# Optimization experiments

Hardware: AMD Instinct MI355X
Metric: run time of the kernel (lower is better)

## Reference

```python
import jax, jax.numpy as jnp
import numpy as np

N_NODES = 100000
N_EDGES = 1600000
IN_C, HID_C, OUT_C = 128, 128, 64


def gcn_conv(x, src, dst, W, b, num_nodes):
    # PyG GCNConv: add self-loops, symmetric normalization, linear transform,
    # aggregate source features into targets.
    h = x @ W  # [N, C_out]
    loop = jnp.arange(num_nodes, dtype=src.dtype)
    s = jnp.concatenate([src, loop])
    d = jnp.concatenate([dst, loop])
    deg = jax.ops.segment_sum(jnp.ones_like(d, dtype=h.dtype), d, num_segments=num_nodes)
    inv_sqrt = jnp.where(deg > 0, jax.lax.rsqrt(deg), 0.0)
    norm = inv_sqrt[s] * inv_sqrt[d]  # [E+N]
    msgs = h[s] * norm[:, None]  # gather + scale
    out = jax.ops.segment_sum(msgs, d, num_segments=num_nodes)  # scatter-add
    return out + b


def setup_inputs() -> dict:
    key = jax.random.key(0)
    k1, k2, k3, k4 = jax.random.split(key, 4)
    x = jax.random.normal(k1, (N_NODES, IN_C), dtype=jnp.float32)
    edge_index = jax.random.randint(k2, (2, N_EDGES), 0, N_NODES, dtype=jnp.int64)
    W1 = jax.random.normal(k3, (IN_C, HID_C), dtype=jnp.float32) * (1.0 / np.sqrt(IN_C))
    b1 = jnp.zeros((HID_C,), dtype=jnp.float32)
    W2 = jax.random.normal(k4, (HID_C, OUT_C), dtype=jnp.float32) * (1.0 / np.sqrt(HID_C))
    b2 = jnp.zeros((OUT_C,), dtype=jnp.float32)
    return {"x": x, "edge_index": edge_index, "W1": W1, "b1": b1, "W2": W2, "b2": b2}


def reference(x, edge_index, W1, b1, W2, b2):
    num_nodes = x.shape[0]
    src, dst = edge_index[0], edge_index[1]  # PyG flow: source -> target
    h = gcn_conv(x, src, dst, W1, b1, num_nodes)
    h = jax.nn.relu(h)  # dropout is identity in eval mode
    out = gcn_conv(h, src, dst, W2, b2, num_nodes)
    return out
```

## Files before the change

kernel.cpp:

```cpp
#include <hip/hip_runtime.h>

#define IN_C 128
#define HID_C 128
#define OUT_C 64

#define BSPAN 256
#define BCAP  5120
#define NBMAX 512
#define ACHUNK 4096

typedef unsigned int uint32;
typedef unsigned short ushort16;
typedef _Float16 f16;
typedef f16   f16x8 __attribute__((ext_vector_type(8)));
typedef float f32x4 __attribute__((ext_vector_type(4)));


__device__ __forceinline__ ushort16 f2bf(float f) {
    union { float f; uint32 u; } v; v.f = f;
    uint32 r = v.u + 0x7FFFu + ((v.u >> 16) & 1u);
    return (ushort16)(r >> 16);
}

__device__ __forceinline__ void unpack2(uint32 u, float& f0, float& f1) {
    union { uint32 x; float f; } a, b;
    a.x = u << 16;
    b.x = u & 0xFFFF0000u;
    f0 = a.f; f1 = b.f;
}

__device__ __forceinline__ void acc_row(uint4 r, float* acc) {
    float f0, f1;
    unpack2(r.x, f0, f1); acc[0] += f0; acc[1] += f1;
    unpack2(r.y, f0, f1); acc[2] += f0; acc[3] += f1;
    unpack2(r.z, f0, f1); acc[4] += f0; acc[5] += f1;
    unpack2(r.w, f0, f1); acc[6] += f0; acc[7] += f1;
}


__launch_bounds__(256)
__global__ void bin_edges_kernel(const int* __restrict__ src, const int* __restrict__ dst,
                                 int* __restrict__ bucketCur, uint32* __restrict__ binned,
                                 int* __restrict__ deg, int E, int nbuck) {
    __shared__ int hist[NBMAX];
    __shared__ int base[NBMAX];
    const int tid = threadIdx.x;
    const int e0  = blockIdx.x * ACHUNK;

    for (int i = tid; i < NBMAX; i += 256) hist[i] = 0;
    __syncthreads();

    int d[16], s[16], rk[16];
#pragma unroll
    for (int j = 0; j < 16; j++) {
        int e = e0 + j * 256 + tid;
        if (e < E) {
            d[j] = dst[e];
            s[j] = src[e];
            rk[j] = atomicAdd(&hist[d[j] >> 8], 1);
            atomicAdd(&deg[d[j]], 1);
        } else d[j] = -1;
    }
    __syncthreads();

    for (int b = tid; b < nbuck; b += 256) {
        int h = hist[b];
        base[b] = h ? atomicAdd(&bucketCur[b], h) : 0;
    }
    __syncthreads();

#pragma unroll
    for (int j = 0; j < 16; j++) {
        if (d[j] >= 0) {
            int b = d[j] >> 8;
            int pos = base[b] + rk[j];
            if (pos < BCAP)
                binned[(size_t)b * BCAP + pos] =
                    ((uint32)(d[j] & 255) << 17) | (uint32)s[j];
        }
    }
}


template <int C>
__device__ __forceinline__ void wprep_one(const float* __restrict__ W, f16* __restrict__ Wf, int t) {
    constexpr int NCT = C / 16;
    int lane = t & 63;
    int ctkc = t >> 6;
    int ct = ctkc % NCT, kc = ctkc / NCT;
    int kbase = kc * 32 + (lane >> 4) * 8;
    int col   = ct * 16 + (lane & 15);
    f16 v[8];
#pragma unroll
    for (int j = 0; j < 8; j++) v[j] = (f16)W[(size_t)(kbase + j) * C + col];
    *(uint4*)(Wf + (size_t)t * 8) = *(const uint4*)v;
}

__global__ void wprep_both(const float* __restrict__ W1, f16* __restrict__ Wf1,
                           const float* __restrict__ W2, f16* __restrict__ Wf2,
                           int* __restrict__ bucketCur, int* __restrict__ deg,
                           int nbuck, int N) {
    constexpr int T1 = 4 * (HID_C / 16) * 64;
    constexpr int T2 = 4 * (OUT_C / 16) * 64;
    int t = blockIdx.x * 256 + threadIdx.x;
    if (t < nbuck) bucketCur[t] = 0;
    if (t < N)     deg[t] = 0;
    if (t < T1)            wprep_one<HID_C>(W1, Wf1, t);
    else if (t < T1 + T2)  wprep_one<OUT_C>(W2, Wf2, t - T1);
}


__launch_bounds__(256)
__global__ void csr_and_gemm(const uint32* __restrict__ binned, const int* __restrict__ bucketCur,
                             int* __restrict__ csr_src, int* __restrict__ rowbeg,
                             int* __restrict__ rowend, float* __restrict__ inv,
                             const float* __restrict__ X, const f16* __restrict__ Wf,
                             const int* __restrict__ deg, ushort16* __restrict__ outb,
                             int N, int ncsr) {
    __shared__ __align__(16) char smem[49152];
    const int tid = threadIdx.x;

    if ((int)blockIdx.x < ncsr) {
        constexpr int MAXIT = BCAP / 256;
        int* cnt  = (int*)smem;
        int* scn  = cnt + BSPAN;
        int* excl = scn + BSPAN;
        const int b   = blockIdx.x;
        const int n0  = b * BSPAN;
        const int ne  = min(bucketCur[b], BCAP);
        const uint32* bp = binned + (size_t)b * BCAP;

        cnt[tid] = 0;
        __syncthreads();

        uint32 ebuf[MAXIT];
        int    rbuf[MAXIT];
        int nmine = 0;
        for (int i = tid; i < ne; i += 256) {
            uint32 e = bp[i];
            ebuf[nmine] = e;
            rbuf[nmine] = atomicAdd(&cnt[e >> 17], 1);
            nmine++;
        }
        __syncthreads();

        int v = cnt[tid];
        scn[tid] = v;
        __syncthreads();
        for (int off = 1; off < 256; off <<= 1) {
            int u = (tid >= off) ? scn[tid - off] : 0;
            __syncthreads();
            scn[tid] += u;
            __syncthreads();
        }
        int ex = scn[tid] - v;
        excl[tid] = ex;

        int n = n0 + tid;
        if (n < N) {
            int gb = b * BCAP + ex;
            rowbeg[n] = gb;
            rowend[n] = gb + v;
            inv[n] = rsqrtf((float)(v + 1));
        }
        __syncthreads();

        for (int j = 0; j < nmine; j++) {
            uint32 e = ebuf[j];
            csr_src[(size_t)b * BCAP + excl[e >> 17] + rbuf[j]] = (int)(e & 0x1FFFFu);
        }
    } else {
        constexpr int C = HID_C;
        constexpr int NCT = C / 16;
        f16* As = (f16*)smem;
        f16* Bs = (f16*)(smem + 16384);

        const int lane = tid & 63;
        const int w    = tid >> 6;
        const int row0 = ((int)blockIdx.x - ncsr) * 64;

        {
            constexpr int TOT = 4 * NCT * 64 * 8;
            const uint4* s = (const uint4*)Wf;
            uint4* d = (uint4*)Bs;
#pragma unroll
            for (int i = 0; i < TOT / 8 / 256; i++)
                d[tid + i * 256] = s[tid + i * 256];
        }

        {
            int r   = tid >> 2;
            int seg = tid & 3;
            int row = row0 + r;
            int ws_ = r >> 4;
            int r15 = r & 15;
#pragma unroll
            for (int i = 0; i < 8; i++) {
                int k = seg * 32 + i * 4;
                float4 v = make_float4(0.f, 0.f, 0.f, 0.f);
                if (row < N) v = *(const float4*)(X + (size_t)row * 128 + k);
                int q = (k >> 3) & 3, j0 = k & 7;
                f16 h[4] = {(f16)v.x, (f16)v.y, (f16)v.z, (f16)v.w};
                int slot = ((seg * 4 + ws_) * 64 + (q * 16 + r15)) * 8 + j0;
                *(uint2*)(As + slot) = *(const uint2*)h;
            }
        }
        __syncthreads();

        f32x4 acc[NCT];
#pragma unroll
        for (int c = 0; c < NCT; c++) acc[c] = (f32x4){0.f, 0.f, 0.f, 0.f};
#pragma unroll
        for (int kc = 0; kc < 4; kc++) {
            f16x8 a = *(const f16x8*)&As[((kc * 4 + w) * 64 + lane) * 8];
#pragma unroll
            for (int ct = 0; ct < NCT; ct++) {
                f16x8 b = *(const f16x8*)&Bs[((kc * NCT + ct) * 64 + lane) * 8];
                acc[ct] = __builtin_amdgcn_mfma_f32_16x16x32_f16(a, b, acc[ct], 0, 0, 0);
            }
        }

        __syncthreads();
        ushort16* Ds = (ushort16*)As;
        const int q = lane >> 4;
        float iv[4];
#pragma unroll
        for (int reg = 0; reg < 4; reg++) {
            int row = row0 + w * 16 + q * 4 + reg;
            iv[reg] = (row < N) ? rsqrtf((float)(deg[row] + 1)) : 0.f;
        }
#pragma unroll
        for (int ct = 0; ct < NCT; ct++) {
#pragma unroll
            for (int reg = 0; reg < 4; reg++) {
                int r = w * 16 + q * 4 + reg;
                Ds[r * C + ct * 16 + (lane & 15)] = f2bf(acc[ct][reg] * iv[reg]);
            }
        }
        __syncthreads();
        {
            int r  = tid >> 2;
            int row = row0 + r;
            if (row < N) {
                constexpr int SPT = C / 4;
                int c0 = (tid & 3) * SPT;
                const uint4* s = (const uint4*)&Ds[r * C + c0];
                uint4* d = (uint4*)(outb + (size_t)row * C + c0);
#pragma unroll
                for (int i = 0; i < SPT / 8; i++) d[i] = s[i];
            }
        }
    }
}


__launch_bounds__(512, 4)
__global__ void fused_gather_gemm(const int* __restrict__ rowbeg, const int* __restrict__ rowend,
                                  const int* __restrict__ csr,
                                  const ushort16* __restrict__ hsb,
                                  const float* __restrict__ inv, const float* __restrict__ bias1,
                                  const f16* __restrict__ Wf2,
                                  ushort16* __restrict__ outb, int N) {
    constexpr int CIN = 128, COUT = 64, NCT = COUT / 16;
    __shared__ __align__(16) f16 As[4 * 4 * 64 * 8];
    __shared__ __align__(16) f16 Bs[4 * NCT * 64 * 8];

    const int tid  = threadIdx.x;
    const int lane = tid & 63;
    const int w    = tid >> 6;
    const int row0 = blockIdx.x * 64;

    {
        const uint4* s = (const uint4*)Wf2;
        uint4* d = (uint4*)Bs;
        d[tid]       = s[tid];
        d[tid + 512] = s[tid + 512];
    }

    {
        const int r = tid >> 3;
        const int q = tid & 7;
        const int n = row0 + r;
        float acc[16];
#pragma unroll
        for (int j = 0; j < 16; j++) acc[j] = 0.f;

        if (n < N) {
            {
                const ushort16* base = hsb + (size_t)n * CIN + q * 16;
                uint4 s0 = *(const uint4*)(base);
                uint4 s1 = *(const uint4*)(base + 8);
                acc_row(s0, acc); acc_row(s1, acc + 8);
            }
            const int end = rowend[n];
            int i = rowbeg[n];
            for (; i + 4 <= end; i += 4) {
                const ushort16* p0 = hsb + (size_t)csr[i]     * CIN + q * 16;
                const ushort16* p1 = hsb + (size_t)csr[i + 1] * CIN + q * 16;
                const ushort16* p2 = hsb + (size_t)csr[i + 2] * CIN + q * 16;
                const ushort16* p3 = hsb + (size_t)csr[i + 3] * CIN + q * 16;
                uint4 a0 = *(const uint4*)(p0);
                uint4 a1 = *(const uint4*)(p0 + 8);
                uint4 b0 = *(const uint4*)(p1);
                uint4 b1 = *(const uint4*)(p1 + 8);
                uint4 c0 = *(const uint4*)(p2);
                uint4 c1 = *(const uint4*)(p2 + 8);
                uint4 d0 = *(const uint4*)(p3);
                uint4 d1 = *(const uint4*)(p3 + 8);
                acc_row(a0, acc); acc_row(a1, acc + 8);
                acc_row(b0, acc); acc_row(b1, acc + 8);
                acc_row(c0, acc); acc_row(c1, acc + 8);
                acc_row(d0, acc); acc_row(d1, acc + 8);
            }
            for (; i < end; i++) {
                const ushort16* p0 = hsb + (size_t)csr[i] * CIN + q * 16;
                uint4 a0 = *(const uint4*)(p0);
                uint4 a1 = *(const uint4*)(p0 + 8);
                acc_row(a0, acc); acc_row(a1, acc + 8);
            }

            float iv = inv[n];
#pragma unroll
            for (int j = 0; j < 16; j++)
                acc[j] = fmaxf(fmaf(iv, acc[j], bias1[q * 16 + j]), 0.f);
        }

        const int ws_ = r >> 4, r15 = r & 15;
        const int seg = q >> 1;
#pragma unroll
        for (int u = 0; u < 2; u++) {
            const int i8 = (q & 1) * 2 + u;
            f16 hv[8];
#pragma unroll
            for (int j = 0; j < 8; j++) hv[j] = (f16)acc[u * 8 + j];
            int slot = ((seg * 4 + ws_) * 64 + (i8 * 16 + r15)) * 8;
            *(uint4*)(As + slot) = *(const uint4*)hv;
        }
    }
    __syncthreads();

    f32x4 acc2[NCT];
#pragma unroll
    for (int c = 0; c < NCT; c++) acc2[c] = (f32x4){0.f, 0.f, 0.f, 0.f};
    if (w < 4) {
#pragma unroll
        for (int kc = 0; kc < 4; kc++) {
            f16x8 a = *(const f16x8*)&As[((kc * 4 + w) * 64 + lane) * 8];
#pragma unroll
            for (int ct = 0; ct < NCT; ct++) {
                f16x8 b = *(const f16x8*)&Bs[((kc * NCT + ct) * 64 + lane) * 8];
                acc2[ct] = __builtin_amdgcn_mfma_f32_16x16x32_f16(a, b, acc2[ct], 0, 0, 0);
            }
        }
    }

    __syncthreads();
    ushort16* Ds = (ushort16*)As;
    if (w < 4) {
        const int q2 = lane >> 4;
        float iv2[4];
#pragma unroll
        for (int reg = 0; reg < 4; reg++) {
            int row = row0 + w * 16 + q2 * 4 + reg;
            iv2[reg] = (row < N) ? inv[row] : 0.f;
        }
#pragma unroll
        for (int ct = 0; ct < NCT; ct++) {
#pragma unroll
            for (int reg = 0; reg < 4; reg++) {
                int r = w * 16 + q2 * 4 + reg;
                Ds[r * COUT + ct * 16 + (lane & 15)] = f2bf(acc2[ct][reg] * iv2[reg]);
            }
        }
    }
    __syncthreads();
    {
        const int r   = tid >> 3;
        const int row = row0 + r;
        if (row < N) {
            const int c0 = (tid & 7) * 8;
            *(uint4*)(outb + (size_t)row * COUT + c0) = *(const uint4*)&Ds[r * COUT + c0];
        }
    }
}


template <int C, bool RELU>
__launch_bounds__(256)
__global__ void gather_agg_bf16(const int* __restrict__ rowbeg, const int* __restrict__ rowend,
                                const int* __restrict__ csr_src,
                                const ushort16* __restrict__ hsb, const float* __restrict__ inv,
                                const float* __restrict__ b, float* __restrict__ out, int N) {
    constexpr int TPN = C / 8;
    constexpr int NPB = 256 / TPN;
    int n    = blockIdx.x * NPB + threadIdx.x / TPN;
    int lane = threadIdx.x % TPN;
    if (n >= N) return;
    int c8 = lane * 8;

    float acc[8];
    {
        uint4 raw = *(const uint4*)(hsb + (size_t)n * C + c8);
        unpack2(raw.x, acc[0], acc[1]);
        unpack2(raw.y, acc[2], acc[3]);
        unpack2(raw.z, acc[4], acc[5]);
        unpack2(raw.w, acc[6], acc[7]);
    }

    int beg = rowbeg[n];
    int end = rowend[n];
    int i = beg;
    for (; i + 4 <= end; i += 4) {
        int s0 = csr_src[i];
        int s1 = csr_src[i + 1];
        int s2 = csr_src[i + 2];
        int s3 = csr_src[i + 3];
        uint4 r0 = *(const uint4*)(hsb + (size_t)s0 * C + c8);
        uint4 r1 = *(const uint4*)(hsb + (size_t)s1 * C + c8);
        uint4 r2 = *(const uint4*)(hsb + (size_t)s2 * C + c8);
        uint4 r3 = *(const uint4*)(hsb + (size_t)s3 * C + c8);
        acc_row(r0, acc); acc_row(r1, acc); acc_row(r2, acc); acc_row(r3, acc);
    }
    for (; i < end; i++) {
        uint4 r0 = *(const uint4*)(hsb + (size_t)csr_src[i] * C + c8);
        acc_row(r0, acc);
    }

    float iv = inv[n];
    float4 b0 = *(const float4*)(b + c8);
    float4 b1 = *(const float4*)(b + c8 + 4);
    float r[8];
    r[0] = fmaf(iv, acc[0], b0.x); r[1] = fmaf(iv, acc[1], b0.y);
    r[2] = fmaf(iv, acc[2], b0.z); r[3] = fmaf(iv, acc[3], b0.w);
    r[4] = fmaf(iv, acc[4], b1.x); r[5] = fmaf(iv, acc[5], b1.y);
    r[6] = fmaf(iv, acc[6], b1.z); r[7] = fmaf(iv, acc[7], b1.w);
    if (RELU) {
#pragma unroll
        for (int j = 0; j < 8; j++) r[j] = fmaxf(r[j], 0.f);
    }
    float* po = out + (size_t)n * C + c8;
    *(float4*)(po)     = make_float4(r[0], r[1], r[2], r[3]);
    *(float4*)(po + 4) = make_float4(r[4], r[5], r[6], r[7]);
}

extern "C" void kernel_launch(void* const* d_in, const int* in_sizes, int n_in,
                              void* d_out, int out_size, void* d_ws, size_t ws_size,
                              hipStream_t stream) {
    const float* x  = (const float*)d_in[0];
    const int*   ei = (const int*)d_in[1];
    const float* W1 = (const float*)d_in[2];
    const float* b1 = (const float*)d_in[3];
    const float* W2 = (const float*)d_in[4];
    const float* b2 = (const float*)d_in[5];
    float* out = (float*)d_out;

    const int N = in_sizes[0] / IN_C;
    const int E = in_sizes[1] / 2;
    const int* src = ei;
    const int* dst = ei + E;
    const int nbuck = (N + BSPAN - 1) / BSPAN;

    char* ws = (char*)d_ws;
    auto align_up = [](size_t v) { return (v + 1023) & ~(size_t)1023; };
    size_t off = 0;
    int*      bucketCur = (int*)(ws + off);      off += align_up((size_t)nbuck * sizeof(int));
    int*      deg       = (int*)(ws + off);      off += align_up((size_t)N * sizeof(int));
    float*    inv       = (float*)(ws + off);    off += align_up((size_t)N * sizeof(float));
    int*      rowbeg    = (int*)(ws + off);      off += align_up((size_t)N * sizeof(int));
    int*      rowend    = (int*)(ws + off);      off += align_up((size_t)N * sizeof(int));
    uint32*   binned    = (uint32*)(ws + off);   off += align_up((size_t)nbuck * BCAP * sizeof(uint32));
    int*      csrs      = (int*)(ws + off);      off += align_up((size_t)nbuck * BCAP * sizeof(int));
    f16*      Wf1       = (f16*)(ws + off);      off += align_up((size_t)4 * (HID_C/16) * 64 * 8 * sizeof(f16));
    f16*      Wf2       = (f16*)(ws + off);      off += align_up((size_t)4 * (OUT_C/16) * 64 * 8 * sizeof(f16));
    ushort16* hs1b      = (ushort16*)(ws + off); off += align_up((size_t)N * HID_C * sizeof(ushort16));
    ushort16* hs2b      = (ushort16*)(ws + off); off += align_up((size_t)N * OUT_C * sizeof(ushort16));

    wprep_both<<<(N + 255) / 256, 256, 0, stream>>>(
        W1, Wf1, W2, Wf2, bucketCur, deg, nbuck, N);

    bin_edges_kernel<<<(E + ACHUNK - 1) / ACHUNK, 256, 0, stream>>>(
        src, dst, bucketCur, binned, deg, E, nbuck);

    {
        const int ngemm = (N + 63) / 64;
        csr_and_gemm<<<nbuck + ngemm, 256, 0, stream>>>(
            binned, bucketCur, csrs, rowbeg, rowend, inv,
            x, Wf1, deg, hs1b, N, nbuck);
    }

    fused_gather_gemm<<<(N + 63) / 64, 512, 0, stream>>>(
        rowbeg, rowend, csrs, hs1b, inv, b1, Wf2, hs2b, N);

    {
        constexpr int NPB = 256 / (OUT_C / 8);
        gather_agg_bf16<OUT_C, false><<<(N + NPB - 1) / NPB, 256, 0, stream>>>(
            rowbeg, rowend, csrs, hs2b, inv, b2, out, N);
    }
}
```

Measured before the change: 304.5 us.

## Replace global degree atomics with per-bucket LDS degree count kernel

The edge-binning kernel no longer issues one global atomicAdd per edge into a degree array. A new deg_inv_kernel instead recounts per-node degrees for each 256-node bucket from the binned edges, using shared-memory atomics, and writes inv directly. The GEMM branch now reads that precomputed inv instead of recomputing rsqrt from deg. Weight preparation is folded into extra blocks of the binning kernel, and the bucket counters are zeroed with a memset. The trade is an extra launch and an extra pass over the binned array in exchange for removing scattered global atomics.

```diff
diff --git a/kernel.cpp b/kernel.cpp
--- a/kernel.cpp
+++ b/kernel.cpp
@@ -35,50 +35,6 @@
     unpack2(r.y, f0, f1); acc[2] += f0; acc[3] += f1;
     unpack2(r.z, f0, f1); acc[4] += f0; acc[5] += f1;
     unpack2(r.w, f0, f1); acc[6] += f0; acc[7] += f1;
-}
-
-
-__launch_bounds__(256)
-__global__ void bin_edges_kernel(const int* __restrict__ src, const int* __restrict__ dst,
-                                 int* __restrict__ bucketCur, uint32* __restrict__ binned,
-                                 int* __restrict__ deg, int E, int nbuck) {
-    __shared__ int hist[NBMAX];
-    __shared__ int base[NBMAX];
-    const int tid = threadIdx.x;
-    const int e0  = blockIdx.x * ACHUNK;
-
-    for (int i = tid; i < NBMAX; i += 256) hist[i] = 0;
-    __syncthreads();
-
-    int d[16], s[16], rk[16];
-#pragma unroll
-    for (int j = 0; j < 16; j++) {
-        int e = e0 + j * 256 + tid;
-        if (e < E) {
-            d[j] = dst[e];
-            s[j] = src[e];
-            rk[j] = atomicAdd(&hist[d[j] >> 8], 1);
-            atomicAdd(&deg[d[j]], 1);
-        } else d[j] = -1;
-    }
-    __syncthreads();
-
-    for (int b = tid; b < nbuck; b += 256) {
-        int h = hist[b];
-        base[b] = h ? atomicAdd(&bucketCur[b], h) : 0;
-    }
-    __syncthreads();
-
-#pragma unroll
-    for (int j = 0; j < 16; j++) {
-        if (d[j] >= 0) {
-            int b = d[j] >> 8;
-            int pos = base[b] + rk[j];
-            if (pos < BCAP)
-                binned[(size_t)b * BCAP + pos] =
-                    ((uint32)(d[j] & 255) << 17) | (uint32)s[j];
-        }
-    }
 }
 
 
@@ -96,26 +52,89 @@
     *(uint4*)(Wf + (size_t)t * 8) = *(const uint4*)v;
 }
 
-__global__ void wprep_both(const float* __restrict__ W1, f16* __restrict__ Wf1,
-                           const float* __restrict__ W2, f16* __restrict__ Wf2,
-                           int* __restrict__ bucketCur, int* __restrict__ deg,
-                           int nbuck, int N) {
-    constexpr int T1 = 4 * (HID_C / 16) * 64;
-    constexpr int T2 = 4 * (OUT_C / 16) * 64;
-    int t = blockIdx.x * 256 + threadIdx.x;
-    if (t < nbuck) bucketCur[t] = 0;
-    if (t < N)     deg[t] = 0;
-    if (t < T1)            wprep_one<HID_C>(W1, Wf1, t);
-    else if (t < T1 + T2)  wprep_one<OUT_C>(W2, Wf2, t - T1);
+
+__launch_bounds__(256)
+__global__ void bin_edges_wprep(const int* __restrict__ src, const int* __restrict__ dst,
+                                int* __restrict__ bucketCur, uint32* __restrict__ binned,
+                                const float* __restrict__ W1, f16* __restrict__ Wf1,
+                                const float* __restrict__ W2, f16* __restrict__ Wf2,
+                                int E, int nbins) {
+    __shared__ int hist[NBMAX];
+    __shared__ int base[NBMAX];
+    const int tid = threadIdx.x;
+
+    if ((int)blockIdx.x >= nbins) {
+        constexpr int T1 = 4 * (HID_C / 16) * 64;
+        constexpr int T2 = 4 * (OUT_C / 16) * 64;
+        int t = ((int)blockIdx.x - nbins) * 256 + tid;
+        if (t < T1)            wprep_one<HID_C>(W1, Wf1, t);
+        else if (t < T1 + T2)  wprep_one<OUT_C>(W2, Wf2, t - T1);
+        return;
+    }
+
+    const int e0 = blockIdx.x * ACHUNK;
+
+    for (int i = tid; i < NBMAX; i += 256) hist[i] = 0;
+    __syncthreads();
+
+    int d[16], s[16], rk[16];
+#pragma unroll
+    for (int j = 0; j < 16; j++) {
+        int e = e0 + j * 256 + tid;
+        if (e < E) {
+            d[j] = dst[e];
+            s[j] = src[e];
+            rk[j] = atomicAdd(&hist[d[j] >> 8], 1);
+        } else d[j] = -1;
+    }
+    __syncthreads();
+
+    for (int b = tid; b < NBMAX; b += 256) {
+        int h = hist[b];
+        base[b] = h ? atomicAdd(&bucketCur[b], h) : 0;
+    }
+    __syncthreads();
+
+#pragma unroll
+    for (int j = 0; j < 16; j++) {
+        if (d[j] >= 0) {
+            int b = d[j] >> 8;
+            int pos = base[b] + rk[j];
+            if (pos < BCAP)
+                binned[(size_t)b * BCAP + pos] =
+                    ((uint32)(d[j] & 255) << 17) | (uint32)s[j];
+        }
+    }
+}
+
+
+__launch_bounds__(256)
+__global__ void deg_inv_kernel(const uint32* __restrict__ binned,
+                               const int* __restrict__ bucketCur,
+                               float* __restrict__ inv, int N) {
+    __shared__ int cnt[BSPAN];
+    const int b   = blockIdx.x;
+    const int tid = threadIdx.x;
+    const int ne  = min(bucketCur[b], BCAP);
+    const uint32* bp = binned + (size_t)b * BCAP;
+
+    cnt[tid] = 0;
+    __syncthreads();
+    for (int i = tid; i < ne; i += 256)
+        atomicAdd(&cnt[bp[i] >> 17], 1);
+    __syncthreads();
+
+    int n = b * BSPAN + tid;
+    if (n < N) inv[n] = rsqrtf((float)(cnt[tid] + 1));
 }
 
 
 __launch_bounds__(256)
 __global__ void csr_and_gemm(const uint32* __restrict__ binned, const int* __restrict__ bucketCur,
                              int* __restrict__ csr_src, int* __restrict__ rowbeg,
-                             int* __restrict__ rowend, float* __restrict__ inv,
+                             int* __restrict__ rowend,
                              const float* __restrict__ X, const f16* __restrict__ Wf,
-                             const int* __restrict__ deg, ushort16* __restrict__ outb,
+                             const float* __restrict__ inv, ushort16* __restrict__ outb,
                              int N, int ncsr) {
     __shared__ __align__(16) char smem[49152];
     const int tid = threadIdx.x;
@@ -161,7 +180,6 @@
             int gb = b * BCAP + ex;
             rowbeg[n] = gb;
             rowend[n] = gb + v;
-            inv[n] = rsqrtf((float)(v + 1));
         }
         __syncthreads();
 
@@ -227,7 +245,7 @@
 #pragma unroll
         for (int reg = 0; reg < 4; reg++) {
             int row = row0 + w * 16 + q * 4 + reg;
-            iv[reg] = (row < N) ? rsqrtf((float)(deg[row] + 1)) : 0.f;
+            iv[reg] = (row < N) ? inv[row] : 0.f;
         }
 #pragma unroll
         for (int ct = 0; ct < NCT; ct++) {
@@ -459,12 +477,12 @@
     const int* src = ei;
     const int* dst = ei + E;
     const int nbuck = (N + BSPAN - 1) / BSPAN;
+    const int nbins = (E + ACHUNK - 1) / ACHUNK;
 
     char* ws = (char*)d_ws;
     auto align_up = [](size_t v) { return (v + 1023) & ~(size_t)1023; };
     size_t off = 0;
     int*      bucketCur = (int*)(ws + off);      off += align_up((size_t)nbuck * sizeof(int));
-    int*      deg       = (int*)(ws + off);      off += align_up((size_t)N * sizeof(int));
     float*    inv       = (float*)(ws + off);    off += align_up((size_t)N * sizeof(float));
     int*      rowbeg    = (int*)(ws + off);      off += align_up((size_t)N * sizeof(int));
     int*      rowend    = (int*)(ws + off);      off += align_up((size_t)N * sizeof(int));
@@ -475,17 +493,21 @@
     ushort16* hs1b      = (ushort16*)(ws + off); off += align_up((size_t)N * HID_C * sizeof(ushort16));
     ushort16* hs2b      = (ushort16*)(ws + off); off += align_up((size_t)N * OUT_C * sizeof(ushort16));
 
-    wprep_both<<<(N + 255) / 256, 256, 0, stream>>>(
-        W1, Wf1, W2, Wf2, bucketCur, deg, nbuck, N);
-
-    bin_edges_kernel<<<(E + ACHUNK - 1) / ACHUNK, 256, 0, stream>>>(
-        src, dst, bucketCur, binned, deg, E, nbuck);
+    hipMemsetAsync(bucketCur, 0, (size_t)nbuck * sizeof(int), stream);
+
+    {
+        constexpr int WPT = 4 * (HID_C / 16 + OUT_C / 16) * 64;
+        bin_edges_wprep<<<nbins + (WPT + 255) / 256, 256, 0, stream>>>(
+            src, dst, bucketCur, binned, W1, Wf1, W2, Wf2, E, nbins);
+    }
+
+    deg_inv_kernel<<<nbuck, 256, 0, stream>>>(binned, bucketCur, inv, N);
 
     {
         const int ngemm = (N + 63) / 64;
         csr_and_gemm<<<nbuck + ngemm, 256, 0, stream>>>(
-            binned, bucketCur, csrs, rowbeg, rowend, inv,
-            x, Wf1, deg, hs1b, N, nbuck);
+            binned, bucketCur, csrs, rowbeg, rowend,
+            x, Wf1, inv, hs1b, N, nbuck);
     }
 
     fused_gather_gemm<<<(N + 63) / 64, 512, 0, stream>>>(
```

New measurement: 257.8 us. 1.18x faster.
